# Kernel optimization log

Measured on AMD Instinct MI355X. Metric: run time of the kernel, lower is better.

Reference implementation:

```python
import jax, jax.numpy as jnp
import numpy as np
import math

D_MODEL = 1024
N_HEAD = 16
D_K = 64
D_V = 64
D_FF = 4096
EPS = 1e-5


def layer_norm(x, g, b):
    m = jnp.mean(x, axis=-1, keepdims=True)
    v = jnp.var(x, axis=-1, keepdims=True)
    return (x - m) * jax.lax.rsqrt(v + EPS) * g + b


def setup_inputs() -> dict:
    key = jax.random.key(0)
    ks = jax.random.split(key, 16)
    B, S, D = 8, 1024, D_MODEL
    s = 0.02
    inp = {
        "x": jax.random.normal(ks[0], (B, S, D), jnp.float32),
        "attn_mask": jnp.zeros((B, 1, 1, S), jnp.bool_),
        "Wq": s * jax.random.normal(ks[1], (D, D), jnp.float32),
        "bq": jnp.zeros((D,), jnp.float32),
        "Wk": s * jax.random.normal(ks[2], (D, D), jnp.float32),
        "bk": jnp.zeros((D,), jnp.float32),
        "Wv": s * jax.random.normal(ks[3], (D, D), jnp.float32),
        "bv": jnp.zeros((D,), jnp.float32),
        "Wo": s * jax.random.normal(ks[4], (D, D), jnp.float32),
        "bo": jnp.zeros((D,), jnp.float32),
        "g1": jnp.ones((D,), jnp.float32),
        "b1": jnp.zeros((D,), jnp.float32),
        "W1": s * jax.random.normal(ks[5], (D_FF, D), jnp.float32),
        "bf1": jnp.zeros((D_FF,), jnp.float32),
        "W2": s * jax.random.normal(ks[6], (D, D_FF), jnp.float32),
        "bf2": jnp.zeros((D,), jnp.float32),
        "Wc": s * jax.random.normal(ks[7], (D, D, 3), jnp.float32),  # (out, in, k)
        "bc": jnp.zeros((D,), jnp.float32),
        "Wf": s * jax.random.normal(ks[8], (D, D), jnp.float32),
        "bf": jnp.zeros((D,), jnp.float32),
        "g2": jnp.ones((D,), jnp.float32),
        "b2": jnp.zeros((D,), jnp.float32),
    }
    return inp


def reference(x, attn_mask, Wq, bq, Wk, bk, Wv, bv, Wo, bo, g1, b1,
              W1, bf1, W2, bf2, Wc, bc, Wf, bf, g2, b2):
    B, S, D = x.shape
    H, dk = N_HEAD, D_K

    # --- Multi-head attention (dropout is eval-mode identity) ---
    q = (x @ Wq.T + bq).reshape(B, S, H, dk)
    k = (x @ Wk.T + bk).reshape(B, S, H, dk)
    v = (x @ Wv.T + bv).reshape(B, S, H, D_V)
    scores = jnp.einsum('bqhd,bkhd->bhqk', q, k) / math.sqrt(dk)
    scores = jnp.where(attn_mask, jnp.float32(-1e9), scores)
    attn = jax.nn.softmax(scores, axis=-1)  # [B,H,S,S]
    ctx = jnp.einsum('bhqk,bkhd->bqhd', attn, v).reshape(B, S, H * D_V)
    proj = ctx @ Wo.T + bo
    # residual is the projected Q (as in the original code)
    attn_out = layer_norm(proj + q.reshape(B, S, D), g1, b1)

    # --- FFN ---
    h = jax.nn.relu(attn_out @ W1.T + bf1) @ W2.T + bf2

    # --- FeatureOptimizationBlock: conv1d(k=3,pad=1) + relu + fc ---
    hc = jax.lax.conv_general_dilated(
        h.transpose(0, 2, 1), Wc, window_strides=(1,), padding='SAME',
        dimension_numbers=('NCH', 'OIH', 'NCH')) + bc[None, :, None]
    hc = jax.nn.relu(hc.transpose(0, 2, 1))
    fob = hc @ Wf.T + bf

    out = layer_norm(fob + attn_out, g2, b2)
    return (out, attn)
```

## Files before the change

### kernel.cpp

```cpp
#include <hip/hip_runtime.h>

#define BATCH 8
#define SEQ   1024
#define DM    1024
#define NH    16
#define DKH   64
#define DFF   4096

typedef short s16x8 __attribute__((ext_vector_type(8)));
typedef float f32x4 __attribute__((ext_vector_type(4)));
typedef unsigned short u16x4 __attribute__((ext_vector_type(4)));
typedef unsigned int u32x4 __attribute__((ext_vector_type(4)));

__device__ __forceinline__ void gload16(const void* g, void* l) {
  __builtin_amdgcn_global_load_lds((const __attribute__((address_space(1))) void*)g,
                                   (__attribute__((address_space(3))) void*)l, 16, 0, 0);
}
__device__ __forceinline__ unsigned short f2b(float f) {
  __bf16 h = (__bf16)f;
  return __builtin_bit_cast(unsigned short, h);
}
__device__ __forceinline__ float b2f(unsigned short u) {
  __bf16 h = __builtin_bit_cast(__bf16, u);
  return (float)h;
}

__global__ __launch_bounds__(256) void cast_kernel(const float* __restrict__ in,
                                                   unsigned short* __restrict__ out, int n4) {
  int i = blockIdx.x * 256 + threadIdx.x;
  if (i < n4) {
    f32x4 v = *(const f32x4*)(in + (size_t)i * 4);
    u16x4 o;
    o[0] = f2b(v[0]); o[1] = f2b(v[1]); o[2] = f2b(v[2]); o[3] = f2b(v[3]);
    *(u16x4*)(out + (size_t)i * 4) = o;
  }
}

__global__ __launch_bounds__(256) void repack_wc_kernel(const float* __restrict__ wc,
                                                        unsigned short* __restrict__ out) {
  int j = blockIdx.x * 256 + threadIdx.x;
  int o = j / 3072;
  int rem = j - o * 3072;
  int i = rem / 3;
  int t = rem - i * 3;
  out[(size_t)o * 3072 + t * 1024 + i] = f2b(wc[j]);
}

__global__ __launch_bounds__(256) void zero_hpad_kernel(unsigned short* __restrict__ hpad) {
  int t = blockIdx.x * 256 + threadIdx.x;
  int b = t >> 11;
  int r = (t >> 10) & 1;
  int c = t & 1023;
  hpad[((size_t)(b * 1026 + r * 1025)) * 1024 + c] = 0;
}

template<bool RELU, bool OUTBF, bool REMAP_A, bool REMAP_O>
__global__ __launch_bounds__(256)
void gemm_bt(const unsigned short* __restrict__ A, const unsigned short* __restrict__ B,
             const float* __restrict__ bias, void* __restrict__ C,
             int N, int K, int lda) {
  __shared__ unsigned short As[128 * 32];
  __shared__ unsigned short Bs[128 * 32];
  const int tid = threadIdx.x;
  const int lane = tid & 63, wave = tid >> 6;
  const int bm = blockIdx.x, bn = blockIdx.y;
  const int wr = (wave >> 1) * 64, wc = (wave & 1) * 64;
  const int l15 = lane & 15, l4 = lane >> 4;

  f32x4 acc[4][4];
  #pragma unroll
  for (int i = 0; i < 4; i++)
    #pragma unroll
    for (int j = 0; j < 4; j++) acc[i][j] = (f32x4){0.f, 0.f, 0.f, 0.f};

  const int r0 = tid >> 2, c0 = (tid & 3) * 8;
  int arow0 = bm * 128 + r0;
  int arow1 = arow0 + 64;
  size_t ga0 = (size_t)(REMAP_A ? arow0 + 2 * (arow0 >> 10) : arow0) * lda + c0;
  size_t ga1 = (size_t)(REMAP_A ? arow1 + 2 * (arow1 >> 10) : arow1) * lda + c0;
  size_t gb0 = (size_t)(bn * 128 + r0) * K + c0;
  size_t gb1 = gb0 + (size_t)64 * K;

  for (int kt = 0; kt < K; kt += 32) {
    gload16(A + ga0 + kt, (char*)As + tid * 16);
    gload16(A + ga1 + kt, (char*)As + 4096 + tid * 16);
    gload16(B + gb0 + kt, (char*)Bs + tid * 16);
    gload16(B + gb1 + kt, (char*)Bs + 4096 + tid * 16);
    __syncthreads();
    s16x8 af[4], bfr[4];
    #pragma unroll
    for (int i = 0; i < 4; i++)
      af[i] = *(const s16x8*)((const char*)As + (wr + i * 16 + l15) * 64 + l4 * 16);
    #pragma unroll
    for (int i = 0; i < 4; i++)
      bfr[i] = *(const s16x8*)((const char*)Bs + (wc + i * 16 + l15) * 64 + l4 * 16);
    #pragma unroll
    for (int i = 0; i < 4; i++)
      #pragma unroll
      for (int j = 0; j < 4; j++)
        acc[i][j] = __builtin_amdgcn_mfma_f32_16x16x32_bf16(af[i], bfr[j], acc[i][j], 0, 0, 0);
    __syncthreads();
  }

  const int crow = bm * 128 + wr + l4 * 4;
  const int ccol = bn * 128 + wc + l15;
  #pragma unroll
  for (int j = 0; j < 4; j++) {
    int col = ccol + j * 16;
    float bv = bias[col];
    #pragma unroll
    for (int i = 0; i < 4; i++) {
      #pragma unroll
      for (int r = 0; r < 4; r++) {
        int row = crow + i * 16 + r;
        float v = acc[i][j][r] + bv;
        if (RELU) v = fmaxf(v, 0.f);
        size_t o = (size_t)(REMAP_O ? row + 2 * (row >> 10) + 1 : row) * N + col;
        if (OUTBF) ((unsigned short*)C)[o] = f2b(v);
        else       ((float*)C)[o] = v;
      }
    }
  }
}

__global__ __launch_bounds__(256)
void transpose_v_kernel(const unsigned short* __restrict__ v, unsigned short* __restrict__ vt) {
  __shared__ unsigned short tile[64][80];
  const int t = threadIdx.x;
  const int st = blockIdx.x * 64, h = blockIdx.y, b = blockIdx.z;
  #pragma unroll
  for (int rep = 0; rep < 2; rep++) {
    int s = (t >> 3) + rep * 32;
    int d0 = (t & 7) * 8;
    u32x4 val = *(const u32x4*)(v + ((size_t)(b * SEQ + st + s)) * DM + h * 64 + d0);
    *(u32x4*)&tile[s][d0] = val;
  }
  __syncthreads();
  #pragma unroll
  for (int rep = 0; rep < 2; rep++) {
    int d = (t >> 3) + rep * 32;
    int s0 = (t & 7) * 8;
    alignas(16) unsigned short tmp[8];
    #pragma unroll
    for (int i = 0; i < 8; i++) tmp[i] = tile[s0 + i][d];
    *(u32x4*)(vt + ((size_t)((b * NH + h) * 64 + d)) * SEQ + st + s0) = *(const u32x4*)tmp;
  }
}

__global__ __launch_bounds__(256, 4)
void attn_kernel(const unsigned short* __restrict__ qb,
                 const unsigned short* __restrict__ kb,
                 const unsigned short* __restrict__ vt,
                 float* __restrict__ attn_out,
                 unsigned short* __restrict__ ctx) {
  __shared__ unsigned short P[16 * 1024];
  __shared__ float redM[4][16];
  __shared__ float redS[4][16];
  const int t = threadIdx.x;
  const int wave = t >> 6, lane = t & 63;
  const int l15 = lane & 15, l4 = lane >> 4;
  const int qt = blockIdx.x, h = blockIdx.y, b = blockIdx.z;
  const int k0 = wave * 256;
  const int sw = (l15 & 7) << 4;

  f32x4 s[16];
  {
    const size_t qrow = (size_t)(b * SEQ + qt * 16 + l15) * DM + h * 64;
    const s16x8 bq0 = *(const s16x8*)(qb + qrow + l4 * 8);
    const s16x8 bq1 = *(const s16x8*)(qb + qrow + 32 + l4 * 8);
    #pragma unroll
    for (int tt = 0; tt < 16; tt++) {
      const unsigned short* kr = kb + (size_t)(b * SEQ + k0 + tt * 16 + l15) * DM + h * 64 + l4 * 8;
      const s16x8 a0 = *(const s16x8*)kr;
      const s16x8 a1 = *(const s16x8*)(kr + 32);
      f32x4 acc = {0.f, 0.f, 0.f, 0.f};
      acc = __builtin_amdgcn_mfma_f32_16x16x32_bf16(a0, bq0, acc, 0, 0, 0);
      acc = __builtin_amdgcn_mfma_f32_16x16x32_bf16(a1, bq1, acc, 0, 0, 0);
      #pragma unroll
      for (int r = 0; r < 4; r++) s[tt][r] = acc[r] * 0.125f;
    }
  }

  float mx = s[0][0];
  #pragma unroll
  for (int tt = 0; tt < 16; tt++)
    #pragma unroll
    for (int r = 0; r < 4; r++) mx = fmaxf(mx, s[tt][r]);
  mx = fmaxf(mx, __shfl_xor(mx, 16));
  mx = fmaxf(mx, __shfl_xor(mx, 32));
  float sum = 0.f;
  #pragma unroll
  for (int tt = 0; tt < 16; tt++)
    #pragma unroll
    for (int r = 0; r < 4; r++) { float e = __expf(s[tt][r] - mx); s[tt][r] = e; sum += e; }
  sum += __shfl_xor(sum, 16);
  sum += __shfl_xor(sum, 32);
  if (lane < 16) { redM[wave][lane] = mx; redS[wave][lane] = sum; }
  __syncthreads();

  float gm = redM[0][l15];
  #pragma unroll
  for (int w = 1; w < 4; w++) gm = fmaxf(gm, redM[w][l15]);
  float gs = 0.f;
  #pragma unroll
  for (int w = 0; w < 4; w++) gs += redS[w][l15] * __expf(redM[w][l15] - gm);
  const float scale = __expf(mx - gm) / gs;

  {
    const size_t ob = ((size_t)((b * NH + h) * SEQ + qt * 16 + l15)) * SEQ + k0 + l4 * 4;
    char* prow = (char*)P + l15 * 2048;
    #pragma unroll
    for (int tt = 0; tt < 16; tt++) {
      f32x4 p;
      #pragma unroll
      for (int r = 0; r < 4; r++) p[r] = s[tt][r] * scale;
      *(f32x4*)(attn_out + ob + tt * 16) = p;
      uint2 pk;
      pk.x = (unsigned int)f2b(p[0]) | ((unsigned int)f2b(p[1]) << 16);
      pk.y = (unsigned int)f2b(p[2]) | ((unsigned int)f2b(p[3]) << 16);
      *(uint2*)(prow + ((((k0 + tt * 16 + l4 * 4) * 2)) ^ sw)) = pk;
    }
  }
  __syncthreads();

  {
    const size_t vrow = (size_t)((b * NH + h) * 64 + wave * 16 + l15) * SEQ;
    const char* prow = (const char*)P + l15 * 2048;
    f32x4 acc0 = {0.f, 0.f, 0.f, 0.f}, acc1 = {0.f, 0.f, 0.f, 0.f};
    #pragma unroll 8
    for (int kc = 0; kc < 32; kc += 2) {
      const s16x8 a0 = *(const s16x8*)(prow + ((kc * 64 + l4 * 16) ^ sw));
      const s16x8 v0 = *(const s16x8*)(vt + vrow + kc * 32 + l4 * 8);
      acc0 = __builtin_amdgcn_mfma_f32_16x16x32_bf16(a0, v0, acc0, 0, 0, 0);
      const s16x8 a1 = *(const s16x8*)(prow + (((kc + 1) * 64 + l4 * 16) ^ sw));
      const s16x8 v1 = *(const s16x8*)(vt + vrow + (kc + 1) * 32 + l4 * 8);
      acc1 = __builtin_amdgcn_mfma_f32_16x16x32_bf16(a1, v1, acc1, 0, 0, 0);
    }
    acc0 = acc0 + acc1;
    #pragma unroll
    for (int r = 0; r < 4; r++) {
      const int row = qt * 16 + l4 * 4 + r;
      const int col = h * 64 + wave * 16 + l15;
      ctx[(size_t)(b * SEQ + row) * DM + col] = f2b(acc0[r]);
    }
  }
}

template<int MODE>
__global__ __launch_bounds__(256)
void ln_kernel(const float* __restrict__ xin, const void* __restrict__ res,
               const float* __restrict__ gamma, const float* __restrict__ beta,
               unsigned short* __restrict__ outb, float* __restrict__ outf) {
  const int row = blockIdx.x, t = threadIdx.x;
  const int lane = t & 63, wave = t >> 6;
  size_t base = (size_t)row * DM + t * 4;
  f32x4 v = *(const f32x4*)(xin + base);
  if (MODE == 0) {
    u16x4 rb = *(const u16x4*)((const unsigned short*)res + base);
    v[0] += b2f(rb[0]); v[1] += b2f(rb[1]); v[2] += b2f(rb[2]); v[3] += b2f(rb[3]);
  } else {
    f32x4 rf = *(const f32x4*)((const float*)res + base);
    v[0] += rf[0]; v[1] += rf[1]; v[2] += rf[2]; v[3] += rf[3];
  }
  float s1 = v[0] + v[1] + v[2] + v[3];
  float s2 = v[0]*v[0] + v[1]*v[1] + v[2]*v[2] + v[3]*v[3];
  #pragma unroll
  for (int off = 32; off; off >>= 1) { s1 += __shfl_xor(s1, off); s2 += __shfl_xor(s2, off); }
  __shared__ float red[8];
  if (lane == 0) { red[wave] = s1; red[4 + wave] = s2; }
  __syncthreads();
  s1 = red[0] + red[1] + red[2] + red[3];
  s2 = red[4] + red[5] + red[6] + red[7];
  float mean = s1 * (1.f / DM);
  float var = s2 * (1.f / DM) - mean * mean;
  float rstd = rsqrtf(var + 1e-5f);
  f32x4 g = *(const f32x4*)(gamma + t * 4);
  f32x4 bb = *(const f32x4*)(beta + t * 4);
  f32x4 o;
  #pragma unroll
  for (int j = 0; j < 4; j++) o[j] = (v[j] - mean) * rstd * g[j] + bb[j];
  if (MODE == 0) {
    u16x4 ob;
    #pragma unroll
    for (int j = 0; j < 4; j++) ob[j] = f2b(o[j]);
    *(u16x4*)(outb + base) = ob;
    *(f32x4*)(outf + base) = o;
  } else {
    *(f32x4*)(outf + base) = o;
  }
}

extern "C" void kernel_launch(void* const* d_in, const int* in_sizes, int n_in,
                              void* d_out, int out_size, void* d_ws, size_t ws_size,
                              hipStream_t stream) {
  (void)in_sizes; (void)n_in; (void)out_size; (void)ws_size;
  const float* x   = (const float*)d_in[0];
  const float* Wq  = (const float*)d_in[2];
  const float* bq  = (const float*)d_in[3];
  const float* Wk  = (const float*)d_in[4];
  const float* bk  = (const float*)d_in[5];
  const float* Wv  = (const float*)d_in[6];
  const float* bv  = (const float*)d_in[7];
  const float* Wo  = (const float*)d_in[8];
  const float* bo  = (const float*)d_in[9];
  const float* g1  = (const float*)d_in[10];
  const float* b1  = (const float*)d_in[11];
  const float* W1  = (const float*)d_in[12];
  const float* bf1 = (const float*)d_in[13];
  const float* W2  = (const float*)d_in[14];
  const float* bf2 = (const float*)d_in[15];
  const float* Wc  = (const float*)d_in[16];
  const float* bc  = (const float*)d_in[17];
  const float* Wf  = (const float*)d_in[18];
  const float* bff = (const float*)d_in[19];
  const float* g2  = (const float*)d_in[20];
  const float* b2  = (const float*)d_in[21];

  char* ws = (char*)d_ws;
  unsigned short* wqb  = (unsigned short*)(ws + 0);
  unsigned short* wkb  = (unsigned short*)(ws + 2097152);
  unsigned short* wvb  = (unsigned short*)(ws + 4194304);
  unsigned short* wob  = (unsigned short*)(ws + 6291456);
  unsigned short* w1b  = (unsigned short*)(ws + 8388608);
  unsigned short* w2b  = (unsigned short*)(ws + 16777216);
  unsigned short* wfb  = (unsigned short*)(ws + 25165824);
  unsigned short* wcrb = (unsigned short*)(ws + 27262976);
  unsigned short* xb   = (unsigned short*)(ws + 33554432);
  unsigned short* qb   = (unsigned short*)(ws + 50331648);
  unsigned short* kb   = (unsigned short*)(ws + 67108864);
  unsigned short* vb   = (unsigned short*)(ws + 83886080);
  unsigned short* vtb  = (unsigned short*)(ws + 100663296);
  float*          proj = (float*)(ws + 117440512);
  unsigned short* aob  = (unsigned short*)(ws + 150994944);
  float*          aof  = (float*)(ws + 167772160);
  unsigned short* hpad = (unsigned short*)(ws + 201326592);
  unsigned short* hc   = (unsigned short*)(ws + 218136576);
  unsigned short* f1   = (unsigned short*)(ws + 50331648);
  unsigned short* ctx  = xb;
  float*          fob  = proj;

  float* out_main = (float*)d_out;
  float* out_attn = (float*)d_out + (size_t)BATCH * SEQ * DM;

  dim3 B256(256);
  cast_kernel<<<8192, B256, 0, stream>>>(x,  xb,  2097152);
  cast_kernel<<<1024, B256, 0, stream>>>(Wq, wqb, 262144);
  cast_kernel<<<1024, B256, 0, stream>>>(Wk, wkb, 262144);
  cast_kernel<<<1024, B256, 0, stream>>>(Wv, wvb, 262144);
  cast_kernel<<<1024, B256, 0, stream>>>(Wo, wob, 262144);
  cast_kernel<<<4096, B256, 0, stream>>>(W1, w1b, 1048576);
  cast_kernel<<<4096, B256, 0, stream>>>(W2, w2b, 1048576);
  cast_kernel<<<1024, B256, 0, stream>>>(Wf, wfb, 262144);
  repack_wc_kernel<<<12288, B256, 0, stream>>>(Wc, wcrb);
  zero_hpad_kernel<<<64, B256, 0, stream>>>(hpad);

  dim3 g64_8(64, 8), g64_32(64, 32);
  gemm_bt<false, true, false, false><<<g64_8, B256, 0, stream>>>(xb, wqb, bq, qb, 1024, 1024, 1024);
  gemm_bt<false, true, false, false><<<g64_8, B256, 0, stream>>>(xb, wkb, bk, kb, 1024, 1024, 1024);
  gemm_bt<false, true, false, false><<<g64_8, B256, 0, stream>>>(xb, wvb, bv, vb, 1024, 1024, 1024);
  transpose_v_kernel<<<dim3(16, 16, 8), B256, 0, stream>>>(vb, vtb);
  attn_kernel<<<dim3(64, 16, 8), B256, 0, stream>>>(qb, kb, vtb, out_attn, ctx);
  gemm_bt<false, false, false, false><<<g64_8, B256, 0, stream>>>(ctx, wob, bo, proj, 1024, 1024, 1024);
  ln_kernel<0><<<8192, B256, 0, stream>>>(proj, qb, g1, b1, aob, aof);
  gemm_bt<true, true, false, false><<<g64_32, B256, 0, stream>>>(aob, w1b, bf1, f1, 4096, 1024, 1024);
  gemm_bt<false, true, false, true><<<g64_8, B256, 0, stream>>>(f1, w2b, bf2, hpad, 1024, 4096, 4096);
  gemm_bt<true, true, true, false><<<g64_8, B256, 0, stream>>>(hpad, wcrb, bc, hc, 1024, 3072, 1024);
  gemm_bt<false, false, false, false><<<g64_8, B256, 0, stream>>>(hc, wfb, bff, fob, 1024, 1024, 1024);
  ln_kernel<1><<<8192, B256, 0, stream>>>(fob, aof, g2, b2, nullptr, out_main);
}
```

Measured before the change: 901.5 us.

## Fuse QKV projection into one GEMM, swizzle block order, prefetch K/V in attention

Merges the Q, K and V weight casts into one cast kernel and runs a single N=3072 GEMM into an interleaved qkv buffer with concatenated biases. The attention, transpose and first layernorm kernels now read from that strided buffer. Adds XCD-style block-index swizzling to the GEMM and the attention grid. Attention gets software-prefetched K and V register rings to hide global load latency. The goals are fewer launches, better L2 locality across chiplets, and overlapped loads, at the cost of more registers and a strided qkv layout.

Result: faster. 883.7 us (-2.0%).

```diff
diff --git a/kernel.cpp b/kernel.cpp
--- a/kernel.cpp
+++ b/kernel.cpp
@@ -34,6 +34,29 @@
     o[0] = f2b(v[0]); o[1] = f2b(v[1]); o[2] = f2b(v[2]); o[3] = f2b(v[3]);
     *(u16x4*)(out + (size_t)i * 4) = o;
   }
+}
+
+__global__ __launch_bounds__(256) void cast4_kernel(const float* __restrict__ a,
+                                                    const float* __restrict__ b,
+                                                    const float* __restrict__ c,
+                                                    const float* __restrict__ d,
+                                                    unsigned short* __restrict__ out) {
+  int i = blockIdx.x * 256 + threadIdx.x;
+  int which = i >> 18;
+  int off = i & 262143;
+  const float* src = which == 0 ? a : which == 1 ? b : which == 2 ? c : d;
+  f32x4 v = *(const f32x4*)(src + (size_t)off * 4);
+  u16x4 o;
+  o[0] = f2b(v[0]); o[1] = f2b(v[1]); o[2] = f2b(v[2]); o[3] = f2b(v[3]);
+  *(u16x4*)(out + (size_t)i * 4) = o;
+}
+
+__global__ __launch_bounds__(256) void bcat_kernel(const float* __restrict__ a,
+                                                   const float* __restrict__ b,
+                                                   const float* __restrict__ c,
+                                                   float* __restrict__ out) {
+  int i = blockIdx.x * 256 + threadIdx.x;
+  out[i] = i < 1024 ? a[i] : i < 2048 ? b[i - 1024] : c[i - 2048];
 }
 
 __global__ __launch_bounds__(256) void repack_wc_kernel(const float* __restrict__ wc,
@@ -63,7 +86,11 @@
   __shared__ unsigned short Bs[128 * 32];
   const int tid = threadIdx.x;
   const int lane = tid & 63, wave = tid >> 6;
-  const int bm = blockIdx.x, bn = blockIdx.y;
+  const int gdy = gridDim.y;
+  const int lin = blockIdx.x * gdy + blockIdx.y;
+  const int ntot = gridDim.x * gdy;
+  const int swz = (lin & 7) * (ntot >> 3) + (lin >> 3);
+  const int bm = swz / gdy, bn = swz - bm * gdy;
   const int wr = (wave >> 1) * 64, wc = (wave & 1) * 64;
   const int l15 = lane & 15, l4 = lane >> 4;
 
@@ -124,7 +151,7 @@
 }
 
 __global__ __launch_bounds__(256)
-void transpose_v_kernel(const unsigned short* __restrict__ v, unsigned short* __restrict__ vt) {
+void transpose_v_kernel(const unsigned short* __restrict__ qkv, unsigned short* __restrict__ vt) {
   __shared__ unsigned short tile[64][80];
   const int t = threadIdx.x;
   const int st = blockIdx.x * 64, h = blockIdx.y, b = blockIdx.z;
@@ -132,7 +159,7 @@
   for (int rep = 0; rep < 2; rep++) {
     int s = (t >> 3) + rep * 32;
     int d0 = (t & 7) * 8;
-    u32x4 val = *(const u32x4*)(v + ((size_t)(b * SEQ + st + s)) * DM + h * 64 + d0);
+    u32x4 val = *(const u32x4*)(qkv + ((size_t)(b * SEQ + st + s)) * 3072 + 2048 + h * 64 + d0);
     *(u32x4*)&tile[s][d0] = val;
   }
   __syncthreads();
@@ -148,8 +175,7 @@
 }
 
 __global__ __launch_bounds__(256, 4)
-void attn_kernel(const unsigned short* __restrict__ qb,
-                 const unsigned short* __restrict__ kb,
+void attn_kernel(const unsigned short* __restrict__ qkv,
                  const unsigned short* __restrict__ vt,
                  float* __restrict__ attn_out,
                  unsigned short* __restrict__ ctx) {
@@ -159,20 +185,32 @@
   const int t = threadIdx.x;
   const int wave = t >> 6, lane = t & 63;
   const int l15 = lane & 15, l4 = lane >> 4;
-  const int qt = blockIdx.x, h = blockIdx.y, b = blockIdx.z;
+  const int id = blockIdx.x;
+  const int swz = (id & 7) * 1024 + (id >> 3);
+  const int qt = swz & 63, h = (swz >> 6) & 15, b = swz >> 10;
   const int k0 = wave * 256;
   const int sw = (l15 & 7) << 4;
 
   f32x4 s[16];
   {
-    const size_t qrow = (size_t)(b * SEQ + qt * 16 + l15) * DM + h * 64;
-    const s16x8 bq0 = *(const s16x8*)(qb + qrow + l4 * 8);
-    const s16x8 bq1 = *(const s16x8*)(qb + qrow + 32 + l4 * 8);
+    const size_t qrow = (size_t)(b * SEQ + qt * 16 + l15) * 3072 + h * 64;
+    const s16x8 bq0 = *(const s16x8*)(qkv + qrow + l4 * 8);
+    const s16x8 bq1 = *(const s16x8*)(qkv + qrow + 32 + l4 * 8);
+    const unsigned short* krow = qkv + (size_t)(b * SEQ + k0 + l15) * 3072 + 1024 + h * 64 + l4 * 8;
+    const size_t kstep = (size_t)16 * 3072;
+    s16x8 pa[4], pb[4];
+    #pragma unroll
+    for (int i = 0; i < 4; i++) {
+      pa[i] = *(const s16x8*)(krow + i * kstep);
+      pb[i] = *(const s16x8*)(krow + i * kstep + 32);
+    }
     #pragma unroll
     for (int tt = 0; tt < 16; tt++) {
-      const unsigned short* kr = kb + (size_t)(b * SEQ + k0 + tt * 16 + l15) * DM + h * 64 + l4 * 8;
-      const s16x8 a0 = *(const s16x8*)kr;
-      const s16x8 a1 = *(const s16x8*)(kr + 32);
+      const s16x8 a0 = pa[tt & 3], a1 = pb[tt & 3];
+      if (tt < 12) {
+        pa[tt & 3] = *(const s16x8*)(krow + (tt + 4) * kstep);
+        pb[tt & 3] = *(const s16x8*)(krow + (tt + 4) * kstep + 32);
+      }
       f32x4 acc = {0.f, 0.f, 0.f, 0.f};
       acc = __builtin_amdgcn_mfma_f32_16x16x32_bf16(a0, bq0, acc, 0, 0, 0);
       acc = __builtin_amdgcn_mfma_f32_16x16x32_bf16(a1, bq1, acc, 0, 0, 0);
@@ -225,16 +263,19 @@
 
   {
     const size_t vrow = (size_t)((b * NH + h) * 64 + wave * 16 + l15) * SEQ;
+    const unsigned short* vbase = vt + vrow + l4 * 8;
     const char* prow = (const char*)P + l15 * 2048;
+    s16x8 vv[4];
+    #pragma unroll
+    for (int i = 0; i < 4; i++) vv[i] = *(const s16x8*)(vbase + i * 32);
     f32x4 acc0 = {0.f, 0.f, 0.f, 0.f}, acc1 = {0.f, 0.f, 0.f, 0.f};
-    #pragma unroll 8
-    for (int kc = 0; kc < 32; kc += 2) {
-      const s16x8 a0 = *(const s16x8*)(prow + ((kc * 64 + l4 * 16) ^ sw));
-      const s16x8 v0 = *(const s16x8*)(vt + vrow + kc * 32 + l4 * 8);
-      acc0 = __builtin_amdgcn_mfma_f32_16x16x32_bf16(a0, v0, acc0, 0, 0, 0);
-      const s16x8 a1 = *(const s16x8*)(prow + (((kc + 1) * 64 + l4 * 16) ^ sw));
-      const s16x8 v1 = *(const s16x8*)(vt + vrow + (kc + 1) * 32 + l4 * 8);
-      acc1 = __builtin_amdgcn_mfma_f32_16x16x32_bf16(a1, v1, acc1, 0, 0, 0);
+    #pragma unroll
+    for (int kc = 0; kc < 32; kc++) {
+      const s16x8 a = *(const s16x8*)(prow + ((kc * 64 + l4 * 16) ^ sw));
+      const s16x8 v0 = vv[kc & 3];
+      if (kc < 28) vv[kc & 3] = *(const s16x8*)(vbase + (kc + 4) * 32);
+      if (kc & 1) acc1 = __builtin_amdgcn_mfma_f32_16x16x32_bf16(a, v0, acc1, 0, 0, 0);
+      else        acc0 = __builtin_amdgcn_mfma_f32_16x16x32_bf16(a, v0, acc0, 0, 0, 0);
     }
     acc0 = acc0 + acc1;
     #pragma unroll
@@ -250,13 +291,14 @@
 __global__ __launch_bounds__(256)
 void ln_kernel(const float* __restrict__ xin, const void* __restrict__ res,
                const float* __restrict__ gamma, const float* __restrict__ beta,
-               unsigned short* __restrict__ outb, float* __restrict__ outf) {
+               unsigned short* __restrict__ outb, float* __restrict__ outf,
+               int rstride) {
   const int row = blockIdx.x, t = threadIdx.x;
   const int lane = t & 63, wave = t >> 6;
   size_t base = (size_t)row * DM + t * 4;
   f32x4 v = *(const f32x4*)(xin + base);
   if (MODE == 0) {
-    u16x4 rb = *(const u16x4*)((const unsigned short*)res + base);
+    u16x4 rb = *(const u16x4*)((const unsigned short*)res + (size_t)row * rstride + t * 4);
     v[0] += b2f(rb[0]); v[1] += b2f(rb[1]); v[2] += b2f(rb[2]); v[3] += b2f(rb[3]);
   } else {
     f32x4 rf = *(const f32x4*)((const float*)res + base);
@@ -318,17 +360,13 @@
 
   char* ws = (char*)d_ws;
   unsigned short* wqb  = (unsigned short*)(ws + 0);
-  unsigned short* wkb  = (unsigned short*)(ws + 2097152);
-  unsigned short* wvb  = (unsigned short*)(ws + 4194304);
   unsigned short* wob  = (unsigned short*)(ws + 6291456);
   unsigned short* w1b  = (unsigned short*)(ws + 8388608);
   unsigned short* w2b  = (unsigned short*)(ws + 16777216);
   unsigned short* wfb  = (unsigned short*)(ws + 25165824);
   unsigned short* wcrb = (unsigned short*)(ws + 27262976);
   unsigned short* xb   = (unsigned short*)(ws + 33554432);
-  unsigned short* qb   = (unsigned short*)(ws + 50331648);
-  unsigned short* kb   = (unsigned short*)(ws + 67108864);
-  unsigned short* vb   = (unsigned short*)(ws + 83886080);
+  unsigned short* qkv  = (unsigned short*)(ws + 50331648);
   unsigned short* vtb  = (unsigned short*)(ws + 100663296);
   float*          proj = (float*)(ws + 117440512);
   unsigned short* aob  = (unsigned short*)(ws + 150994944);
@@ -336,6 +374,7 @@
   unsigned short* hpad = (unsigned short*)(ws + 201326592);
   unsigned short* hc   = (unsigned short*)(ws + 218136576);
   unsigned short* f1   = (unsigned short*)(ws + 50331648);
+  float*          bqkv = (float*)(ws + 234913792);
   unsigned short* ctx  = xb;
   float*          fob  = proj;
 
@@ -344,27 +383,23 @@
 
   dim3 B256(256);
   cast_kernel<<<8192, B256, 0, stream>>>(x,  xb,  2097152);
-  cast_kernel<<<1024, B256, 0, stream>>>(Wq, wqb, 262144);
-  cast_kernel<<<1024, B256, 0, stream>>>(Wk, wkb, 262144);
-  cast_kernel<<<1024, B256, 0, stream>>>(Wv, wvb, 262144);
-  cast_kernel<<<1024, B256, 0, stream>>>(Wo, wob, 262144);
+  cast4_kernel<<<4096, B256, 0, stream>>>(Wq, Wk, Wv, Wo, wqb);
   cast_kernel<<<4096, B256, 0, stream>>>(W1, w1b, 1048576);
   cast_kernel<<<4096, B256, 0, stream>>>(W2, w2b, 1048576);
   cast_kernel<<<1024, B256, 0, stream>>>(Wf, wfb, 262144);
   repack_wc_kernel<<<12288, B256, 0, stream>>>(Wc, wcrb);
   zero_hpad_kernel<<<64, B256, 0, stream>>>(hpad);
-
-  dim3 g64_8(64, 8), g64_32(64, 32);
-  gemm_bt<false, true, false, false><<<g64_8, B256, 0, stream>>>(xb, wqb, bq, qb, 1024, 1024, 1024);
-  gemm_bt<false, true, false, false><<<g64_8, B256, 0, stream>>>(xb, wkb, bk, kb, 1024, 1024, 1024);
-  gemm_bt<false, true, false, false><<<g64_8, B256, 0, stream>>>(xb, wvb, bv, vb, 1024, 1024, 1024);
-  transpose_v_kernel<<<dim3(16, 16, 8), B256, 0, stream>>>(vb, vtb);
-  attn_kernel<<<dim3(64, 16, 8), B256, 0, stream>>>(qb, kb, vtb, out_attn, ctx);
+  bcat_kernel<<<12, B256, 0, stream>>>(bq, bk, bv, bqkv);
+
+  dim3 g64_8(64, 8), g64_24(64, 24), g64_32(64, 32);
+  gemm_bt<false, true, false, false><<<g64_24, B256, 0, stream>>>(xb, wqb, bqkv, qkv, 3072, 1024, 1024);
+  transpose_v_kernel<<<dim3(16, 16, 8), B256, 0, stream>>>(qkv, vtb);
+  attn_kernel<<<dim3(8192), B256, 0, stream>>>(qkv, vtb, out_attn, ctx);
   gemm_bt<false, false, false, false><<<g64_8, B256, 0, stream>>>(ctx, wob, bo, proj, 1024, 1024, 1024);
-  ln_kernel<0><<<8192, B256, 0, stream>>>(proj, qb, g1, b1, aob, aof);
+  ln_kernel<0><<<8192, B256, 0, stream>>>(proj, qkv, g1, b1, aob, aof, 3072);
   gemm_bt<true, true, false, false><<<g64_32, B256, 0, stream>>>(aob, w1b, bf1, f1, 4096, 1024, 1024);
   gemm_bt<false, true, false, true><<<g64_8, B256, 0, stream>>>(f1, w2b, bf2, hpad, 1024, 4096, 4096);
   gemm_bt<true, true, true, false><<<g64_8, B256, 0, stream>>>(hpad, wcrb, bc, hc, 1024, 3072, 1024);
   gemm_bt<false, false, false, false><<<g64_8, B256, 0, stream>>>(hc, wfb, bff, fob, 1024, 1024, 1024);
-  ln_kernel<1><<<8192, B256, 0, stream>>>(fob, aof, g2, b2, nullptr, out_main);
-}
+  ln_kernel<1><<<8192, B256, 0, stream>>>(fob, aof, g2, b2, nullptr, out_main, 1024);
+}
```
